# Performance work log

Hardware: AMD Instinct MI355X
Metric: run time of the kernel (lower is better)

Reference implementation:

```python
import jax, jax.numpy as jnp
import numpy as np

DECAY = 0.99
EPS = 1e-05
N_EMBED = 512
DIM = 64


def setup_inputs() -> dict:
    key = jax.random.key(0)
    k1, k2, k3 = jax.random.split(key, 3)
    x = jax.random.normal(k1, (32, DIM, 64, 64), dtype=jnp.float32)  # NCHW
    dictionary = jax.random.normal(k2, (DIM, N_EMBED), dtype=jnp.float32)
    cluster_size = jnp.zeros((N_EMBED,), dtype=jnp.float32)
    dictionary_avg = jax.random.normal(k3, (DIM, N_EMBED), dtype=jnp.float32)
    return {"x": x, "dictionary": dictionary, "cluster_size": cluster_size,
            "dictionary_avg": dictionary_avg}


def reference(x, dictionary, cluster_size, dictionary_avg):
    B, C, H, W = x.shape
    permuted = jnp.transpose(x, (0, 2, 3, 1))            # [B,H,W,dim]
    flatten = permuted.reshape(-1, C)                     # [N,dim]

    # pairwise squared distances: ||f||^2 - 2 f.D + ||D||^2  -> [N, n_embed]
    dist = (jnp.sum(flatten * flatten, axis=1, keepdims=True)
            - 2.0 * flatten @ dictionary
            + jnp.sum(dictionary * dictionary, axis=0, keepdims=True))
    embed_ind_flat = jnp.argmax(-dist, axis=1)            # [N] int
    embed_ind = embed_ind_flat.reshape(B, H, W)

    # codebook lookup (gather of dictionary columns)
    quantize = jnp.take(dictionary.T, embed_ind, axis=0)  # [B,H,W,dim]

    # EMA codebook update (training-mode buffer math), scatter via segment_sum
    counts = jax.ops.segment_sum(jnp.ones_like(embed_ind_flat, dtype=flatten.dtype),
                                 embed_ind_flat, num_segments=N_EMBED)
    new_cluster_size = DECAY * cluster_size + (1.0 - DECAY) * counts
    embed_sum = jax.ops.segment_sum(flatten, embed_ind_flat,
                                    num_segments=N_EMBED).T  # [dim, n_embed]
    new_dictionary_avg = DECAY * dictionary_avg + (1.0 - DECAY) * embed_sum
    n = jnp.sum(new_cluster_size)
    cs = (new_cluster_size + EPS) / (n + N_EMBED * EPS) * n
    new_dictionary = new_dictionary_avg / cs[None, :]

    diff = jnp.mean((jax.lax.stop_gradient(quantize) - permuted) ** 2)
    quantize_st = permuted + jax.lax.stop_gradient(quantize - permuted)
    out = jnp.transpose(quantize_st, (0, 3, 1, 2))        # back to NCHW
    mean_D = jnp.mean(jnp.abs(new_dictionary))
    return out, diff, embed_ind, new_cluster_size, new_dictionary_avg, new_dictionary, mean_D
```

## Files before the change

kernel.cpp:

```cpp
#include <hip/hip_runtime.h>
#include <math.h>

#define DIMC 64
#define NE 512
#define HWSZ 4096
#define NPTS 131072
#define DECAYF 0.99f
#define OMD 0.01f
#define EPSF 1e-5f
#define MARGIN 1e-3f

#define O0 0
#define O1 8388608
#define O2 8388609
#define O3 8519681
#define O4 8520193
#define O5 8552961
#define O6 8585729

#define WS_DIFF   0
#define WS_ESUM   64
#define WS_COUNTS 32832
#define WS_DT     33344
#define WS_NORM   66112
#define WS_DHI    66624
#define WS_DLO    83008
#define WS_PART   246852
#define PART_STRIDE 33280
#define NBLK 256
#define WS_NEED_BYTES ((size_t)(WS_PART + (size_t)NBLK * PART_STRIDE) * 4)

typedef __attribute__((ext_vector_type(8))) short bf16x8;
typedef __attribute__((ext_vector_type(4))) float f32x4;

__device__ __forceinline__ unsigned bf16rne(float x) {
    unsigned u = __float_as_uint(x);
    return (u + 0x7FFFu + ((u >> 16) & 1u)) >> 16;
}

__global__ void k_prep(const float* __restrict__ dict, float* __restrict__ ws) {
    int j = blockIdx.x, c = threadIdx.x;
    float v = dict[c * NE + j];
    ws[WS_DT + j * DIMC + c] = v;
    unsigned h = bf16rne(v);
    float fh = __uint_as_float(h << 16);
    unsigned l = bf16rne(v - fh);
    ((unsigned short*)(ws + WS_DHI))[j * DIMC + c] = (unsigned short)h;
    ((unsigned short*)(ws + WS_DLO))[j * DIMC + c] = (unsigned short)l;
    ws[WS_ESUM + j * DIMC + c] = 0.f;
    if (c == 0) ws[WS_COUNTS + j] = 0.f;
    if (j == 0 && c == 0) ws[WS_DIFF] = 0.f;
    float s = v * v;
    #pragma unroll
    for (int off = 32; off > 0; off >>= 1) s += __shfl_down(s, off);
    if (c == 0) ws[WS_NORM + j] = -0.5f * s;
}

#define MFMA16(A, B, C) __builtin_amdgcn_mfma_f32_16x16x32_bf16(A, B, C, 0, 0, 0)

__global__ __launch_bounds__(512, 1) void k_main(
        const float* __restrict__ x, float* __restrict__ ws,
        float* __restrict__ out, int use_part) {
    extern __shared__ float lds[];
    char*  ldsB   = (char*)lds;
    float* esum   = lds;
    int*   lhist  = (int*)(lds + 32768);
    int*   bidxl  = (int*)(lds + 33280);
    int*   lflist = (int*)(lds + 33792);
    int*   lcnt   = (int*)(lds + 34304);
    float* lred   = lds + 34308;

    const int tid  = threadIdx.x;
    const int lane = tid & 63;
    const int w    = tid >> 6;

    const int nb = blockIdx.x * 512;
    const int n0 = nb + tid;
    const int b = n0 >> 12, hw0 = n0 & 4095;
    const float* xp = x + (size_t)b * (DIMC * HWSZ) + hw0;

    float f0[DIMC];
    #pragma unroll
    for (int c = 0; c < DIMC; ++c) f0[c] = xp[c * HWSZ];
    {
        unsigned hiw[32], low[32];
        #pragma unroll
        for (int i = 0; i < 32; ++i) {
            unsigned h0 = bf16rne(f0[2 * i]);
            unsigned h1 = bf16rne(f0[2 * i + 1]);
            float fh0 = __uint_as_float(h0 << 16);
            float fh1 = __uint_as_float(h1 << 16);
            unsigned l0 = bf16rne(f0[2 * i] - fh0);
            unsigned l1 = bf16rne(f0[2 * i + 1] - fh1);
            hiw[i] = h0 | (h1 << 16);
            low[i] = l0 | (l1 << 16);
        }
        const int swz = tid & 7;
        #pragma unroll
        for (int k = 0; k < 8; ++k) {
            uint4 vh = {hiw[4 * k], hiw[4 * k + 1], hiw[4 * k + 2], hiw[4 * k + 3]};
            uint4 vl = {low[4 * k], low[4 * k + 1], low[4 * k + 2], low[4 * k + 3]};
            *(uint4*)(ldsB + tid * 128 + ((k ^ swz) << 4)) = vh;
            *(uint4*)(ldsB + 65536 + tid * 128 + ((k ^ swz) << 4)) = vl;
        }
    }
    lhist[tid] = 0;
    if (tid == 0) lcnt[0] = 0;
    __syncthreads();

    bf16x8 ahi[4][2], alo[4][2];
    #pragma unroll
    for (int pt = 0; pt < 4; ++pt) {
        const int arow = (w << 6) + (pt << 4) + (lane & 15);
        const int swz = arow & 7;
        #pragma unroll
        for (int kk = 0; kk < 2; ++kk) {
            const int ch = (lane >> 4) + (kk << 2);
            ahi[pt][kk] = __builtin_bit_cast(bf16x8,
                *(const uint4*)(ldsB + arow * 128 + ((ch ^ swz) << 4)));
            alo[pt][kk] = __builtin_bit_cast(bf16x8,
                *(const uint4*)(ldsB + 65536 + arow * 128 + ((ch ^ swz) << 4)));
        }
    }
    __syncthreads();

    {
        float4 z = {0.f, 0.f, 0.f, 0.f};
        float4* e4 = (float4*)lds;
        #pragma unroll
        for (int k = 0; k < 16; ++k) e4[tid + 512 * k] = z;
    }

    const uint4* dh4 = (const uint4*)(ws + WS_DHI);
    const uint4* dl4 = (const uint4*)(ws + WS_DLO);
    const float* npl = ws + WS_NORM + (lane & 15);
    const int bl = ((lane & 15) << 3) + (lane >> 4);

    float best[4][4], sec[4][4];
    int   idx[4][4];
    #pragma unroll
    for (int pt = 0; pt < 4; ++pt)
        #pragma unroll
        for (int r = 0; r < 4; ++r) {
            best[pt][r] = -3.4e38f; sec[pt][r] = -3.4e38f; idx[pt][r] = 0;
        }

    #pragma unroll 2
    for (int jt = 0; jt < 32; ++jt) {
        uint4 uh0 = dh4[(jt << 7) + bl];
        uint4 uh1 = dh4[(jt << 7) + bl + 4];
        uint4 ul0 = dl4[(jt << 7) + bl];
        uint4 ul1 = dl4[(jt << 7) + bl + 4];
        float nrm = npl[jt << 4];
        bf16x8 bh0 = __builtin_bit_cast(bf16x8, uh0);
        bf16x8 bh1 = __builtin_bit_cast(bf16x8, uh1);
        bf16x8 bl0 = __builtin_bit_cast(bf16x8, ul0);
        bf16x8 bl1 = __builtin_bit_cast(bf16x8, ul1);
        const int jc = (jt << 4) + (lane & 15);
        #pragma unroll
        for (int pt = 0; pt < 4; ++pt) {
            f32x4 acc = {0.f, 0.f, 0.f, 0.f};
            acc = MFMA16(ahi[pt][0], bh0, acc);
            acc = MFMA16(ahi[pt][1], bh1, acc);
            acc = MFMA16(ahi[pt][0], bl0, acc);
            acc = MFMA16(ahi[pt][1], bl1, acc);
            acc = MFMA16(alo[pt][0], bh0, acc);
            acc = MFMA16(alo[pt][1], bh1, acc);
            acc = MFMA16(alo[pt][0], bl0, acc);
            acc = MFMA16(alo[pt][1], bl1, acc);
            #pragma unroll
            for (int r = 0; r < 4; ++r) {
                float s = acc[r] + nrm;
                bool gt = s > best[pt][r];
                float ns = gt ? best[pt][r] : (s > sec[pt][r] ? s : sec[pt][r]);
                best[pt][r] = gt ? s : best[pt][r];
                idx[pt][r]  = gt ? jc : idx[pt][r];
                sec[pt][r]  = ns;
            }
        }
    }

    #pragma unroll
    for (int off = 8; off > 0; off >>= 1) {
        #pragma unroll
        for (int pt = 0; pt < 4; ++pt)
            #pragma unroll
            for (int r = 0; r < 4; ++r) {
                float ob = __shfl_xor(best[pt][r], off, 16);
                float os = __shfl_xor(sec[pt][r], off, 16);
                int   oi = __shfl_xor(idx[pt][r], off, 16);
                bool take = (ob > best[pt][r]) ||
                            (ob == best[pt][r] && oi < idx[pt][r]);
                float nsec = fmaxf(fminf(ob, best[pt][r]),
                                   fmaxf(os, sec[pt][r]));
                best[pt][r] = take ? ob : best[pt][r];
                idx[pt][r]  = take ? oi : idx[pt][r];
                sec[pt][r]  = nsec;
            }
    }
    if ((lane & 15) == 0) {
        const int g = lane >> 4;
        #pragma unroll
        for (int pt = 0; pt < 4; ++pt)
            #pragma unroll
            for (int r = 0; r < 4; ++r) {
                int p = (w << 6) + (pt << 4) + (g << 2) + r;
                int flag = (best[pt][r] - sec[pt][r] < MARGIN) ? 65536 : 0;
                bidxl[p] = idx[pt][r] | flag;
            }
    }
    __syncthreads();

    {
        int e = bidxl[tid];
        if (e & 65536) {
            int pos = atomicAdd(lcnt, 1);
            lflist[pos] = tid;
        }
    }
    __syncthreads();

    const float* dptr = ws + WS_DT;
    {
        const int nf = lcnt[0];
        const int hwb = nb & 4095;
        for (int fi = w; fi < nf; fi += 8) {
            const int pp = lflist[fi];
            const float xv = x[(size_t)b * (DIMC * HWSZ)
                               + (size_t)lane * HWSZ + hwb + pp];
            float bb = -3.4e38f; int bj = 0;
            #pragma unroll 2
            for (int s = 0; s < 8; ++s) {
                const int j = (lane << 3) + s;
                const float4* row = (const float4*)(dptr + (size_t)j * DIMC);
                float a0 = 0.f, a1 = 0.f, a2 = 0.f, a3 = 0.f;
                #pragma unroll
                for (int c4 = 0; c4 < 16; ++c4) {
                    float4 r4 = row[c4];
                    a0 = fmaf(r4.x, __shfl(xv, 4 * c4 + 0), a0);
                    a1 = fmaf(r4.y, __shfl(xv, 4 * c4 + 1), a1);
                    a2 = fmaf(r4.z, __shfl(xv, 4 * c4 + 2), a2);
                    a3 = fmaf(r4.w, __shfl(xv, 4 * c4 + 3), a3);
                }
                float sc = ((a0 + a1) + (a2 + a3)) + ws[WS_NORM + j];
                if (sc > bb) { bb = sc; bj = j; }
            }
            #pragma unroll
            for (int off = 1; off < 64; off <<= 1) {
                float ob = __shfl_xor(bb, off);
                int   oi = __shfl_xor(bj, off);
                bool take = (ob > bb) || (ob == bb && oi < bj);
                bb = take ? ob : bb;
                bj = take ? oi : bj;
            }
            if (lane == 0) bidxl[pp] = bj;
        }
    }
    __syncthreads();

    const int bi0 = bidxl[tid] & 511;
    atomicAdd(&lhist[bi0], 1);
    out[O2 + n0] = (float)bi0;

    float ssum = 0.f;
    float* o0 = out + O0 + (size_t)b * (DIMC * HWSZ) + hw0;
    const float4* q40 = (const float4*)(dptr + (size_t)bi0 * DIMC);
    #pragma unroll
    for (int c4 = 0; c4 < 16; ++c4) {
        float4 qa = q40[c4];
        const int cb = 4 * c4;
        o0[(cb + 0) * HWSZ] = qa.x;
        o0[(cb + 1) * HWSZ] = qa.y;
        o0[(cb + 2) * HWSZ] = qa.z;
        o0[(cb + 3) * HWSZ] = qa.w;
        float d;
        d = qa.x - f0[cb + 0]; ssum = fmaf(d, d, ssum);
        d = qa.y - f0[cb + 1]; ssum = fmaf(d, d, ssum);
        d = qa.z - f0[cb + 2]; ssum = fmaf(d, d, ssum);
        d = qa.w - f0[cb + 3]; ssum = fmaf(d, d, ssum);
    }

    #pragma unroll
    for (int c = 0; c < DIMC; ++c) atomicAdd(&esum[c * NE + bi0], f0[c]);
    __syncthreads();

    if (use_part) {
        float* part = ws + WS_PART + (size_t)blockIdx.x * PART_STRIDE;
        float4* p4 = (float4*)part;
        const float4* e4 = (const float4*)esum;
        #pragma unroll
        for (int k = 0; k < 16; ++k) p4[tid + 512 * k] = e4[tid + 512 * k];
        part[32768 + tid] = (float)lhist[tid];
    } else {
        #pragma unroll
        for (int k = 0; k < 64; ++k)
            atomicAdd(&ws[WS_ESUM + tid + 512 * k], esum[tid + 512 * k]);
        atomicAdd(&ws[WS_COUNTS + tid], (float)lhist[tid]);
    }

    #pragma unroll
    for (int off = 32; off > 0; off >>= 1) ssum += __shfl_down(ssum, off);
    if ((tid & 63) == 0) lred[tid >> 6] = ssum;
    __syncthreads();
    if (tid == 0) {
        float t = 0.f;
        #pragma unroll
        for (int w2 = 0; w2 < 8; ++w2) t += lred[w2];
        atomicAdd(ws + WS_DIFF, t);
    }
}

__global__ void k_reduce(float* __restrict__ ws) {
    const int gid = blockIdx.x * 128 + threadIdx.x;
    const float4* src = (const float4*)(ws + WS_PART);
    float4 acc = {0.f, 0.f, 0.f, 0.f};
    #pragma unroll 4
    for (int p = 0; p < NBLK; ++p) {
        float4 v = src[(size_t)p * (PART_STRIDE / 4) + gid];
        acc.x += v.x; acc.y += v.y; acc.z += v.z; acc.w += v.w;
    }
    ((float4*)(ws + WS_ESUM))[gid] = acc;
}

__global__ void k_final(const float* __restrict__ ws,
                        const float* __restrict__ cluster_size,
                        const float* __restrict__ davg,
                        float* __restrict__ out) {
    __shared__ float red[16];
    __shared__ float nsh;
    const int j = threadIdx.x;

    float cnt = ws[WS_COUNTS + j];
    float ncs = DECAYF * cluster_size[j] + OMD * cnt;
    out[O3 + j] = ncs;

    float v = ncs;
    #pragma unroll
    for (int off = 32; off > 0; off >>= 1) v += __shfl_down(v, off);
    if ((j & 63) == 0) red[j >> 6] = v;
    __syncthreads();
    if (j == 0) {
        float t = 0.f;
        #pragma unroll
        for (int w = 0; w < 8; ++w) t += red[w];
        nsh = t;
    }
    __syncthreads();
    const float n = nsh;
    const float csj = (ncs + EPSF) / (n + NE * EPSF) * n;

    float asum = 0.f;
    #pragma unroll
    for (int c = 0; c < DIMC; ++c) {
        float es = ws[WS_ESUM + c * NE + j];
        float da = davg[c * NE + j];
        float nda = DECAYF * da + OMD * es;
        out[O4 + c * NE + j] = nda;
        float nd = nda / csj;
        out[O5 + c * NE + j] = nd;
        asum += fabsf(nd);
    }

    __syncthreads();
    #pragma unroll
    for (int off = 32; off > 0; off >>= 1) asum += __shfl_down(asum, off);
    if ((j & 63) == 0) red[j >> 6] = asum;
    __syncthreads();
    if (j == 0) {
        float t = 0.f;
        #pragma unroll
        for (int w = 0; w < 8; ++w) t += red[w];
        out[O6] = t / 32768.0f;
        out[O1] = ws[WS_DIFF] / 8388608.0f;
    }
}

extern "C" void kernel_launch(void* const* d_in, const int* in_sizes, int n_in,
                              void* d_out, int out_size, void* d_ws, size_t ws_size,
                              hipStream_t stream) {
    const float* x    = (const float*)d_in[0];
    const float* dict = (const float*)d_in[1];
    const float* csz  = (const float*)d_in[2];
    const float* davg = (const float*)d_in[3];
    float* out = (float*)d_out;
    float* ws  = (float*)d_ws;

    const int use_part = (ws_size >= WS_NEED_BYTES) ? 1 : 0;

    k_prep<<<512, 64, 0, stream>>>(dict, ws);

    const int main_lds = 34320 * 4;
    hipFuncSetAttribute((const void*)k_main,
                        hipFuncAttributeMaxDynamicSharedMemorySize, main_lds);
    k_main<<<NBLK, 512, main_lds, stream>>>(x, ws, out, use_part);

    if (use_part) k_reduce<<<65, 128, 0, stream>>>(ws);

    k_final<<<1, 512, 0, stream>>>(ws, csz, davg, out);
}
```

Measured before the change: 146.9 us.

## Split main kernel into high-occupancy scoring kernel and separate emit kernel

The monolithic k_main (256 blocks of 512 threads, one block per CU, large LDS) is split in two. k_score runs 1024 blocks of 256 threads with small static LDS and writes per-point best indices to workspace. k_emit then re-reads x to do the histogram, the embed-sum scatter, the output write and the diff sum. k_reduce is also split four ways across partition slices and combined with atomics. The aim is more concurrent waves on the MFMA distance loop across the 256 CUs. In exchange x is read twice, there is an extra launch, and the reduce now relies on WS_ESUM being zeroed by k_prep.

```diff
diff --git a/kernel.cpp b/kernel.cpp
--- a/kernel.cpp
+++ b/kernel.cpp
@@ -25,6 +25,7 @@
 #define WS_NORM   66112
 #define WS_DHI    66624
 #define WS_DLO    83008
+#define WS_BIDX   99392
 #define WS_PART   246852
 #define PART_STRIDE 33280
 #define NBLK 256
@@ -58,88 +59,85 @@
 
 #define MFMA16(A, B, C) __builtin_amdgcn_mfma_f32_16x16x32_bf16(A, B, C, 0, 0, 0)
 
-__global__ __launch_bounds__(512, 1) void k_main(
-        const float* __restrict__ x, float* __restrict__ ws,
-        float* __restrict__ out, int use_part) {
-    extern __shared__ float lds[];
-    char*  ldsB   = (char*)lds;
-    float* esum   = lds;
-    int*   lhist  = (int*)(lds + 32768);
-    int*   bidxl  = (int*)(lds + 33280);
-    int*   lflist = (int*)(lds + 33792);
-    int*   lcnt   = (int*)(lds + 34304);
-    float* lred   = lds + 34308;
+__global__ __launch_bounds__(256, 4) void k_score(
+        const float* __restrict__ x, float* __restrict__ ws) {
+    __shared__ char stg[16384];
+    __shared__ int bidxl[128];
+    __shared__ int lflist[128];
+    __shared__ int lcnt;
 
     const int tid  = threadIdx.x;
     const int lane = tid & 63;
     const int w    = tid >> 6;
 
-    const int nb = blockIdx.x * 512;
-    const int n0 = nb + tid;
-    const int b = n0 >> 12, hw0 = n0 & 4095;
-    const float* xp = x + (size_t)b * (DIMC * HWSZ) + hw0;
-
-    float f0[DIMC];
-    #pragma unroll
-    for (int c = 0; c < DIMC; ++c) f0[c] = xp[c * HWSZ];
-    {
-        unsigned hiw[32], low[32];
-        #pragma unroll
-        for (int i = 0; i < 32; ++i) {
-            unsigned h0 = bf16rne(f0[2 * i]);
-            unsigned h1 = bf16rne(f0[2 * i + 1]);
-            float fh0 = __uint_as_float(h0 << 16);
-            float fh1 = __uint_as_float(h1 << 16);
-            unsigned l0 = bf16rne(f0[2 * i] - fh0);
-            unsigned l1 = bf16rne(f0[2 * i + 1] - fh1);
-            hiw[i] = h0 | (h1 << 16);
-            low[i] = l0 | (l1 << 16);
-        }
-        const int swz = tid & 7;
-        #pragma unroll
-        for (int k = 0; k < 8; ++k) {
-            uint4 vh = {hiw[4 * k], hiw[4 * k + 1], hiw[4 * k + 2], hiw[4 * k + 3]};
-            uint4 vl = {low[4 * k], low[4 * k + 1], low[4 * k + 2], low[4 * k + 3]};
-            *(uint4*)(ldsB + tid * 128 + ((k ^ swz) << 4)) = vh;
-            *(uint4*)(ldsB + 65536 + tid * 128 + ((k ^ swz) << 4)) = vl;
-        }
-    }
-    lhist[tid] = 0;
-    if (tid == 0) lcnt[0] = 0;
-    __syncthreads();
-
-    bf16x8 ahi[4][2], alo[4][2];
-    #pragma unroll
-    for (int pt = 0; pt < 4; ++pt) {
-        const int arow = (w << 6) + (pt << 4) + (lane & 15);
-        const int swz = arow & 7;
+    const int nb  = blockIdx.x * 128;
+    const int b   = nb >> 12;
+    const int hwb = nb & 4095;
+
+    if (tid == 0) lcnt = 0;
+
+    const int p = tid & 127, h = tid >> 7;
+    const float* xp = x + (size_t)b * (DIMC * HWSZ) + (size_t)(32 * h) * HWSZ
+                        + hwb + p;
+    unsigned hiu[16], lou[16];
+    #pragma unroll
+    for (int i = 0; i < 16; ++i) {
+        float v0 = xp[(2 * i) * HWSZ];
+        float v1 = xp[(2 * i + 1) * HWSZ];
+        unsigned h0 = bf16rne(v0), h1 = bf16rne(v1);
+        float r0 = v0 - __uint_as_float(h0 << 16);
+        float r1 = v1 - __uint_as_float(h1 << 16);
+        hiu[i] = h0 | (h1 << 16);
+        lou[i] = bf16rne(r0) | (bf16rne(r1) << 16);
+    }
+    const int swz = p & 7;
+    #pragma unroll
+    for (int k = 0; k < 4; ++k) {
+        uint4 u = {hiu[4 * k], hiu[4 * k + 1], hiu[4 * k + 2], hiu[4 * k + 3]};
+        *(uint4*)(stg + p * 128 + (((4 * h + k) ^ swz) << 4)) = u;
+    }
+    __syncthreads();
+
+    bf16x8 ahi[2][2], alo[2][2];
+    #pragma unroll
+    for (int pt = 0; pt < 2; ++pt) {
+        const int row = (w << 5) + (pt << 4) + (lane & 15);
         #pragma unroll
         for (int kk = 0; kk < 2; ++kk) {
             const int ch = (lane >> 4) + (kk << 2);
             ahi[pt][kk] = __builtin_bit_cast(bf16x8,
-                *(const uint4*)(ldsB + arow * 128 + ((ch ^ swz) << 4)));
+                *(const uint4*)(stg + row * 128 + ((ch ^ (row & 7)) << 4)));
+        }
+    }
+    __syncthreads();
+
+    #pragma unroll
+    for (int k = 0; k < 4; ++k) {
+        uint4 u = {lou[4 * k], lou[4 * k + 1], lou[4 * k + 2], lou[4 * k + 3]};
+        *(uint4*)(stg + p * 128 + (((4 * h + k) ^ swz) << 4)) = u;
+    }
+    __syncthreads();
+    #pragma unroll
+    for (int pt = 0; pt < 2; ++pt) {
+        const int row = (w << 5) + (pt << 4) + (lane & 15);
+        #pragma unroll
+        for (int kk = 0; kk < 2; ++kk) {
+            const int ch = (lane >> 4) + (kk << 2);
             alo[pt][kk] = __builtin_bit_cast(bf16x8,
-                *(const uint4*)(ldsB + 65536 + arow * 128 + ((ch ^ swz) << 4)));
-        }
-    }
-    __syncthreads();
-
-    {
-        float4 z = {0.f, 0.f, 0.f, 0.f};
-        float4* e4 = (float4*)lds;
-        #pragma unroll
-        for (int k = 0; k < 16; ++k) e4[tid + 512 * k] = z;
-    }
+                *(const uint4*)(stg + row * 128 + ((ch ^ (row & 7)) << 4)));
+        }
+    }
+    __syncthreads();
 
     const uint4* dh4 = (const uint4*)(ws + WS_DHI);
     const uint4* dl4 = (const uint4*)(ws + WS_DLO);
     const float* npl = ws + WS_NORM + (lane & 15);
     const int bl = ((lane & 15) << 3) + (lane >> 4);
 
-    float best[4][4], sec[4][4];
-    int   idx[4][4];
-    #pragma unroll
-    for (int pt = 0; pt < 4; ++pt)
+    float best[2][4], sec[2][4];
+    int   idx[2][4];
+    #pragma unroll
+    for (int pt = 0; pt < 2; ++pt)
         #pragma unroll
         for (int r = 0; r < 4; ++r) {
             best[pt][r] = -3.4e38f; sec[pt][r] = -3.4e38f; idx[pt][r] = 0;
@@ -158,7 +156,7 @@
         bf16x8 bl1 = __builtin_bit_cast(bf16x8, ul1);
         const int jc = (jt << 4) + (lane & 15);
         #pragma unroll
-        for (int pt = 0; pt < 4; ++pt) {
+        for (int pt = 0; pt < 2; ++pt) {
             f32x4 acc = {0.f, 0.f, 0.f, 0.f};
             acc = MFMA16(ahi[pt][0], bh0, acc);
             acc = MFMA16(ahi[pt][1], bh1, acc);
@@ -183,7 +181,7 @@
     #pragma unroll
     for (int off = 8; off > 0; off >>= 1) {
         #pragma unroll
-        for (int pt = 0; pt < 4; ++pt)
+        for (int pt = 0; pt < 2; ++pt)
             #pragma unroll
             for (int r = 0; r < 4; ++r) {
                 float ob = __shfl_xor(best[pt][r], off, 16);
@@ -201,20 +199,20 @@
     if ((lane & 15) == 0) {
         const int g = lane >> 4;
         #pragma unroll
-        for (int pt = 0; pt < 4; ++pt)
+        for (int pt = 0; pt < 2; ++pt)
             #pragma unroll
             for (int r = 0; r < 4; ++r) {
-                int p = (w << 6) + (pt << 4) + (g << 2) + r;
+                int pp = (w << 5) + (pt << 4) + (g << 2) + r;
                 int flag = (best[pt][r] - sec[pt][r] < MARGIN) ? 65536 : 0;
-                bidxl[p] = idx[pt][r] | flag;
+                bidxl[pp] = idx[pt][r] | flag;
             }
     }
     __syncthreads();
 
-    {
+    if (tid < 128) {
         int e = bidxl[tid];
         if (e & 65536) {
-            int pos = atomicAdd(lcnt, 1);
+            int pos = atomicAdd(&lcnt, 1);
             lflist[pos] = tid;
         }
     }
@@ -222,9 +220,8 @@
 
     const float* dptr = ws + WS_DT;
     {
-        const int nf = lcnt[0];
-        const int hwb = nb & 4095;
-        for (int fi = w; fi < nf; fi += 8) {
+        const int nf = lcnt;
+        for (int fi = w; fi < nf; fi += 4) {
             const int pp = lflist[fi];
             const float xv = x[(size_t)b * (DIMC * HWSZ)
                                + (size_t)lane * HWSZ + hwb + pp];
@@ -258,13 +255,74 @@
     }
     __syncthreads();
 
-    const int bi0 = bidxl[tid] & 511;
+    if (tid < 128) ((int*)ws)[WS_BIDX + nb + tid] = bidxl[tid] & 511;
+}
+
+__global__ __launch_bounds__(512, 1) void k_emit(
+        const float* __restrict__ x, float* __restrict__ ws,
+        float* __restrict__ out, int use_part) {
+    extern __shared__ float lds[];
+    float* esum  = lds;
+    int*   lhist = (int*)(lds + 32768);
+    float* lred  = lds + 33280;
+
+    const int tid = threadIdx.x;
+    {
+        float4 z = {0.f, 0.f, 0.f, 0.f};
+        float4* e4 = (float4*)esum;
+        #pragma unroll
+        for (int k = 0; k < 16; ++k) e4[tid + 512 * k] = z;
+        lhist[tid] = 0;
+    }
+    __syncthreads();
+
+    const int n0 = blockIdx.x * 512 + tid;
+    const int b = n0 >> 12, hw0 = n0 & 4095;
+    const float* xp = x + (size_t)b * (DIMC * HWSZ) + hw0;
+    float f0[DIMC];
+    #pragma unroll
+    for (int c = 0; c < DIMC; ++c) f0[c] = xp[c * HWSZ];
+
+    const int bi0 = ((const int*)ws)[WS_BIDX + n0];
     atomicAdd(&lhist[bi0], 1);
+
+    #pragma unroll
+    for (int c = 0; c < DIMC; ++c) atomicAdd(&esum[c * NE + bi0], f0[c]);
+
+    const float* dptr = ws + WS_DT;
+    float ssum = 0.f;
+    const float4* q40 = (const float4*)(dptr + (size_t)bi0 * DIMC);
+    #pragma unroll
+    for (int c4 = 0; c4 < 16; ++c4) {
+        float4 qa = q40[c4];
+        const int cb = 4 * c4;
+        float d;
+        d = qa.x - f0[cb + 0]; ssum = fmaf(d, d, ssum);
+        d = qa.y - f0[cb + 1]; ssum = fmaf(d, d, ssum);
+        d = qa.z - f0[cb + 2]; ssum = fmaf(d, d, ssum);
+        d = qa.w - f0[cb + 3]; ssum = fmaf(d, d, ssum);
+    }
+    #pragma unroll
+    for (int off = 32; off > 0; off >>= 1) ssum += __shfl_down(ssum, off);
+    if ((tid & 63) == 0) lred[tid >> 6] = ssum;
+    __syncthreads();
+
+    if (use_part) {
+        float* part = ws + WS_PART + (size_t)blockIdx.x * PART_STRIDE;
+        float4* p4 = (float4*)part;
+        const float4* e4 = (const float4*)esum;
+        #pragma unroll
+        for (int k = 0; k < 16; ++k) p4[tid + 512 * k] = e4[tid + 512 * k];
+        part[32768 + tid] = (float)lhist[tid];
+    } else {
+        #pragma unroll
+        for (int k = 0; k < 64; ++k)
+            atomicAdd(&ws[WS_ESUM + tid + 512 * k], esum[tid + 512 * k]);
+        atomicAdd(&ws[WS_COUNTS + tid], (float)lhist[tid]);
+    }
+
     out[O2 + n0] = (float)bi0;
-
-    float ssum = 0.f;
     float* o0 = out + O0 + (size_t)b * (DIMC * HWSZ) + hw0;
-    const float4* q40 = (const float4*)(dptr + (size_t)bi0 * DIMC);
     #pragma unroll
     for (int c4 = 0; c4 < 16; ++c4) {
         float4 qa = q40[c4];
@@ -273,35 +331,8 @@
         o0[(cb + 1) * HWSZ] = qa.y;
         o0[(cb + 2) * HWSZ] = qa.z;
         o0[(cb + 3) * HWSZ] = qa.w;
-        float d;
-        d = qa.x - f0[cb + 0]; ssum = fmaf(d, d, ssum);
-        d = qa.y - f0[cb + 1]; ssum = fmaf(d, d, ssum);
-        d = qa.z - f0[cb + 2]; ssum = fmaf(d, d, ssum);
-        d = qa.w - f0[cb + 3]; ssum = fmaf(d, d, ssum);
-    }
-
-    #pragma unroll
-    for (int c = 0; c < DIMC; ++c) atomicAdd(&esum[c * NE + bi0], f0[c]);
-    __syncthreads();
-
-    if (use_part) {
-        float* part = ws + WS_PART + (size_t)blockIdx.x * PART_STRIDE;
-        float4* p4 = (float4*)part;
-        const float4* e4 = (const float4*)esum;
-        #pragma unroll
-        for (int k = 0; k < 16; ++k) p4[tid + 512 * k] = e4[tid + 512 * k];
-        part[32768 + tid] = (float)lhist[tid];
-    } else {
-        #pragma unroll
-        for (int k = 0; k < 64; ++k)
-            atomicAdd(&ws[WS_ESUM + tid + 512 * k], esum[tid + 512 * k]);
-        atomicAdd(&ws[WS_COUNTS + tid], (float)lhist[tid]);
-    }
-
-    #pragma unroll
-    for (int off = 32; off > 0; off >>= 1) ssum += __shfl_down(ssum, off);
-    if ((tid & 63) == 0) lred[tid >> 6] = ssum;
-    __syncthreads();
+    }
+
     if (tid == 0) {
         float t = 0.f;
         #pragma unroll
@@ -311,15 +342,22 @@
 }
 
 __global__ void k_reduce(float* __restrict__ ws) {
-    const int gid = blockIdx.x * 128 + threadIdx.x;
+    const int tid = threadIdx.x;
+    const int gid = (blockIdx.x % 65) * 128 + tid;
+    const int slice = blockIdx.x / 65;
     const float4* src = (const float4*)(ws + WS_PART);
     float4 acc = {0.f, 0.f, 0.f, 0.f};
+    const int p0 = slice * 64;
     #pragma unroll 4
-    for (int p = 0; p < NBLK; ++p) {
+    for (int p = p0; p < p0 + 64; ++p) {
         float4 v = src[(size_t)p * (PART_STRIDE / 4) + gid];
         acc.x += v.x; acc.y += v.y; acc.z += v.z; acc.w += v.w;
     }
-    ((float4*)(ws + WS_ESUM))[gid] = acc;
+    float* dst = ws + WS_ESUM + gid * 4;
+    atomicAdd(dst + 0, acc.x);
+    atomicAdd(dst + 1, acc.y);
+    atomicAdd(dst + 2, acc.z);
+    atomicAdd(dst + 3, acc.w);
 }
 
 __global__ void k_final(const float* __restrict__ ws,
@@ -389,12 +427,14 @@
 
     k_prep<<<512, 64, 0, stream>>>(dict, ws);
 
-    const int main_lds = 34320 * 4;
-    hipFuncSetAttribute((const void*)k_main,
-                        hipFuncAttributeMaxDynamicSharedMemorySize, main_lds);
-    k_main<<<NBLK, 512, main_lds, stream>>>(x, ws, out, use_part);
-
-    if (use_part) k_reduce<<<65, 128, 0, stream>>>(ws);
+    k_score<<<1024, 256, 0, stream>>>(x, ws);
+
+    const int emit_lds = 33288 * 4;
+    hipFuncSetAttribute((const void*)k_emit,
+                        hipFuncAttributeMaxDynamicSharedMemorySize, emit_lds);
+    k_emit<<<NBLK, 512, emit_lds, stream>>>(x, ws, out, use_part);
+
+    if (use_part) k_reduce<<<260, 128, 0, stream>>>(ws);
 
     k_final<<<1, 512, 0, stream>>>(ws, csz, davg, out);
 }
```

Measured after the change: 169.2 us. 1.15x slower.

## Stage codebook in swizzled LDS and split partial-sum reduction across more blocks

Applied to the files above, without the earlier changes.

The main kernel now copies the bf16 hi/lo codebook tiles from global memory into LDS with an XOR swizzle, and the distance loop reads B fragments from LDS instead of global memory. The esum zeroing moves after the argmax phase so that the same LDS region can hold the codebook first. Separately, k_reduce splits the partial-sum reduction over four slices of 64 blocks, launches 260 blocks and combines the slices with atomicAdd. This raises reduction parallelism, but it assumes NBLK is 256 and that WS_ESUM is zeroed before the reduction.

```diff
diff --git a/kernel.cpp b/kernel.cpp
--- a/kernel.cpp
+++ b/kernel.cpp
@@ -125,16 +125,25 @@
     __syncthreads();
 
     {
-        float4 z = {0.f, 0.f, 0.f, 0.f};
-        float4* e4 = (float4*)lds;
-        #pragma unroll
-        for (int k = 0; k < 16; ++k) e4[tid + 512 * k] = z;
-    }
-
-    const uint4* dh4 = (const uint4*)(ws + WS_DHI);
-    const uint4* dl4 = (const uint4*)(ws + WS_DLO);
-    const float* npl = ws + WS_NORM + (lane & 15);
-    const int bl = ((lane & 15) << 3) + (lane >> 4);
+        const uint4* gdh = (const uint4*)(ws + WS_DHI);
+        const uint4* gdl = (const uint4*)(ws + WS_DLO);
+        uint4* LA = (uint4*)lds;
+        #pragma unroll
+        for (int k = 0; k < 8; ++k) {
+            const int i = k * 512 + tid;
+            const int cl = i >> 3, ch = i & 7;
+            const int dp = cl * 8 + (ch ^ (cl & 7));
+            LA[dp] = gdh[i];
+            LA[4096 + dp] = gdl[i];
+        }
+    }
+    __syncthreads();
+
+    const uint4* Lh = (const uint4*)lds;
+    const uint4* Ll = Lh + 4096;
+    const int col = lane & 15, g = lane >> 4;
+    const int cswz = col & 7;
+    const float* npl = ws + WS_NORM + col;
 
     float best[4][4], sec[4][4];
     int   idx[4][4];
@@ -147,16 +156,17 @@
 
     #pragma unroll 2
     for (int jt = 0; jt < 32; ++jt) {
-        uint4 uh0 = dh4[(jt << 7) + bl];
-        uint4 uh1 = dh4[(jt << 7) + bl + 4];
-        uint4 ul0 = dl4[(jt << 7) + bl];
-        uint4 ul1 = dl4[(jt << 7) + bl + 4];
+        const int base = (jt << 7) + (col << 3);
+        uint4 uh0 = Lh[base + (g ^ cswz)];
+        uint4 uh1 = Lh[base + ((g + 4) ^ cswz)];
+        uint4 ul0 = Ll[base + (g ^ cswz)];
+        uint4 ul1 = Ll[base + ((g + 4) ^ cswz)];
         float nrm = npl[jt << 4];
         bf16x8 bh0 = __builtin_bit_cast(bf16x8, uh0);
         bf16x8 bh1 = __builtin_bit_cast(bf16x8, uh1);
         bf16x8 bl0 = __builtin_bit_cast(bf16x8, ul0);
         bf16x8 bl1 = __builtin_bit_cast(bf16x8, ul1);
-        const int jc = (jt << 4) + (lane & 15);
+        const int jc = (jt << 4) + col;
         #pragma unroll
         for (int pt = 0; pt < 4; ++pt) {
             f32x4 acc = {0.f, 0.f, 0.f, 0.f};
@@ -199,12 +209,12 @@
             }
     }
     if ((lane & 15) == 0) {
-        const int g = lane >> 4;
+        const int gq = lane >> 4;
         #pragma unroll
         for (int pt = 0; pt < 4; ++pt)
             #pragma unroll
             for (int r = 0; r < 4; ++r) {
-                int p = (w << 6) + (pt << 4) + (g << 2) + r;
+                int p = (w << 6) + (pt << 4) + (gq << 2) + r;
                 int flag = (best[pt][r] - sec[pt][r] < MARGIN) ? 65536 : 0;
                 bidxl[p] = idx[pt][r] | flag;
             }
@@ -258,6 +268,14 @@
     }
     __syncthreads();
 
+    {
+        float4 z = {0.f, 0.f, 0.f, 0.f};
+        float4* e4 = (float4*)lds;
+        #pragma unroll
+        for (int k = 0; k < 16; ++k) e4[tid + 512 * k] = z;
+    }
+    __syncthreads();
+
     const int bi0 = bidxl[tid] & 511;
     atomicAdd(&lhist[bi0], 1);
     out[O2 + n0] = (float)bi0;
@@ -311,15 +329,22 @@
 }
 
 __global__ void k_reduce(float* __restrict__ ws) {
-    const int gid = blockIdx.x * 128 + threadIdx.x;
+    const int tid = threadIdx.x;
+    const int gid = (blockIdx.x % 65) * 128 + tid;
+    const int slice = blockIdx.x / 65;
     const float4* src = (const float4*)(ws + WS_PART);
     float4 acc = {0.f, 0.f, 0.f, 0.f};
+    const int p0 = slice * 64;
     #pragma unroll 4
-    for (int p = 0; p < NBLK; ++p) {
+    for (int p = p0; p < p0 + 64; ++p) {
         float4 v = src[(size_t)p * (PART_STRIDE / 4) + gid];
         acc.x += v.x; acc.y += v.y; acc.z += v.z; acc.w += v.w;
     }
-    ((float4*)(ws + WS_ESUM))[gid] = acc;
+    float* dst = ws + WS_ESUM + gid * 4;
+    atomicAdd(dst + 0, acc.x);
+    atomicAdd(dst + 1, acc.y);
+    atomicAdd(dst + 2, acc.z);
+    atomicAdd(dst + 3, acc.w);
 }
 
 __global__ void k_final(const float* __restrict__ ws,
@@ -394,7 +419,7 @@
                         hipFuncAttributeMaxDynamicSharedMemorySize, main_lds);
     k_main<<<NBLK, 512, main_lds, stream>>>(x, ws, out, use_part);
 
-    if (use_part) k_reduce<<<65, 128, 0, stream>>>(ws);
+    if (use_part) k_reduce<<<260, 128, 0, stream>>>(ws);
 
     k_final<<<1, 512, 0, stream>>>(ws, csz, davg, out);
 }
```

Measured after the change: 126.2 us. -14.1%, faster.
